# Optimization experiments

Measured on AMD Instinct MI355X. Metric: run time of the kernel, lower is better.

The kernel has to match this reference:

```python
import jax, jax.numpy as jnp
import numpy as np
from itertools import combinations

BASIS = 16  # identity + sums over every nonempty subset of the 4 set axes


def eq4_layer(x, coefs, bias):
    """Permutation-equivariant 4->4 set layer.
    x: (B, Din, n, n, n, n); coefs: (Din, Dout, 16); bias: (Dout,)
    Basis op 0 is identity; ops 1..15 are sums over each nonempty subset of the
    four set axes, broadcast back to full shape. We never stack the 16 full-size
    ops: pooled ops are contracted in their small (keepdims) form and broadcast-added.
    """
    out = jnp.einsum('ds,bdijkl->bsijkl', coefs[:, :, 0], x)
    b = 1
    for r in range(1, 5):
        for axes in combinations((2, 3, 4, 5), r):
            m = x.sum(axis=axes, keepdims=True)  # small marginal tensor
            out = out + jnp.einsum('ds,bd...->bs...', coefs[:, :, b], m)
            b += 1
    return out + bias.reshape(1, -1, 1, 1, 1, 1)


def setup_inputs() -> dict:
    key = jax.random.key(0)
    ks = jax.random.split(key, 9)
    B, n = 4, 24
    nembed, embed_dim, hid, out_dim = 1000, 15, 16, 16
    D = embed_dim + 1  # 16, = layers[0]
    s = 0.1
    return {
        'xcat': jax.random.randint(ks[0], (B, n), 0, nembed),
        'xfeat': jax.random.normal(ks[1], (B, n), dtype=jnp.float32),
        'embed': jax.random.normal(ks[2], (nembed, embed_dim), dtype=jnp.float32) * s,
        'coefs1': jax.random.normal(ks[3], (D, hid, BASIS), dtype=jnp.float32) * s,
        'bias1': jnp.zeros((hid,), dtype=jnp.float32),
        'coefs2': jax.random.normal(ks[4], (hid, out_dim, BASIS), dtype=jnp.float32) * s,
        'bias2': jnp.zeros((out_dim,), dtype=jnp.float32),
        'w_out': jax.random.normal(ks[5], (1, out_dim), dtype=jnp.float32) * s,
        'b_out': jnp.zeros((1,), dtype=jnp.float32),
    }


def reference(xcat, xfeat, embed, coefs1, bias1, coefs2, bias2, w_out, b_out):
    e = jax.nn.relu(embed[xcat])                       # (B, n, embed_dim)
    x = jnp.concatenate([e, xfeat[..., None]], axis=-1)  # (B, n, D)
    # 4th-order outer product per channel: (B, D, n, n, n, n)
    T = jnp.einsum('bid,bjd,bkd,bld->bdijkl', x, x, x, x)
    T = jax.nn.relu(eq4_layer(T, coefs1, bias1))
    T = jax.nn.relu(eq4_layer(T, coefs2, bias2))
    pooled = T.sum(axis=(2, 3, 4, 5))                  # (B, out_dim)
    return pooled @ w_out.T + b_out                    # (B, 1)
```

## Files before the change

### kernel.cpp

```cpp
#include <hip/hip_runtime.h>
#include <hip/hip_bf16.h>


#define NB 4
#define NN 24
#define ND 16
#define NS 16
#define NO 16
#define NKL 576
#define TSTRIDE 1152

typedef unsigned int u32;
typedef unsigned short u16;

__device__ __forceinline__ u16 f2bf(float f) {
  u32 u = __float_as_uint(f);
  u = (u + 0x7fffu + ((u >> 16) & 1u)) >> 16;
  return (u16)u;
}
__device__ __forceinline__ float bflo(u32 u) { return __uint_as_float(u << 16); }
__device__ __forceinline__ float bfhi(u32 u) { return __uint_as_float(u & 0xffff0000u); }

__global__ __launch_bounds__(256) void kt_tables(
    const int* __restrict__ xcat, const float* __restrict__ xfeat,
    const float* __restrict__ embed,
    const float* __restrict__ coefs1, const float* __restrict__ bias1,
    float* __restrict__ tabs) {
  const int blk = blockIdx.x;
  const int j = blk % NN, i = (blk / NN) % NN, b = blk / (NN * NN);
  const int t = threadIdx.x;
  __shared__ float sx[NN * ND];
  __shared__ float SwL[16];
  __shared__ float Af[256], tb[256], tg[256], td[256];
  __shared__ float dconst[16];
  for (int idx = t; idx < NN * ND; idx += 256) {
    int d = idx & 15, ii = idx >> 4;
    float v;
    if (d < 15) v = fmaxf(embed[xcat[b * NN + ii] * 15 + d], 0.f);
    else        v = xfeat[b * NN + ii];
    sx[idx] = v;
  }
  __syncthreads();
  if (t < 16) {
    float s = 0.f;
    for (int ii = 0; ii < NN; ++ii) s += sx[ii * 16 + t];
    SwL[t] = s;
  }
  __syncthreads();
  {
    int d = t >> 4, s = t & 15;
    const float* c = coefs1 + t * 16;
    float xi = sx[i * 16 + d], xj = sx[j * 16 + d];
    float Sv = SwL[d];
    float S2 = Sv * Sv, S3 = S2 * Sv, S4 = S2 * S2, pij = xi * xj;
    Af[s * 16 + d] = c[0] * pij + c[1] * Sv * xj + c[2] * Sv * xi + c[5] * S2;
    tb[t] = c[4] * Sv * pij + c[9] * S2 * xi + c[7] * S2 * xj + c[12] * S3;
    tg[t] = c[3] * Sv * pij + c[8] * S2 * xi + c[6] * S2 * xj + c[11] * S3;
    td[t] = c[10] * S2 * pij + c[14] * S3 * xi + c[13] * S3 * xj + c[15] * S4;
  }
  __syncthreads();
  if (t < 16) {
    float sd = 0.f;
    for (int d = 0; d < 16; ++d) sd += td[d * 16 + t];
    dconst[t] = sd + bias1[t];
  }
  __syncthreads();
  float* tile = tabs + (size_t)blk * TSTRIDE;
  if (t < 128) {
    int s = t >> 3, m = t & 7;
    tile[t] = __uint_as_float((u32)f2bf(Af[s * 16 + 2 * m]) |
                              ((u32)f2bf(Af[s * 16 + 2 * m + 1]) << 16));
  }
  for (int idx = t; idx < 768; idx += 256) {
    int pos = idx >> 4, s = idx & 15;
    if (pos < NN) {
      float acc = 0.f;
#pragma unroll
      for (int d = 0; d < 16; ++d) acc += tb[d * 16 + s] * sx[pos * 16 + d];
      tile[128 + s * 32 + (pos / 3) * 4 + pos % 3] = acc;
    } else {
      int l = pos - NN;
      float acc = dconst[s];
#pragma unroll
      for (int d = 0; d < 16; ++d) acc += tg[d * 16 + s] * sx[l * 16 + d];
      tile[640 + s * 32 + (l / 3) * 4 + l % 3] = acc;
    }
  }
}

__global__ __launch_bounds__(192, 2) void kb_eval(
    const int* __restrict__ xcat, const float* __restrict__ xfeat,
    const float* __restrict__ embed, const float* __restrict__ coefs2,
    const float* __restrict__ tabs,
    u32* __restrict__ T1g, u32* __restrict__ mkc_p, u32* __restrict__ mlc_p,
    u32* __restrict__ mklc_p) {
  const int blk = blockIdx.x;
  const int b = blk / (NN * NN);
  const int t = threadIdx.x;
  __shared__ float sx[NN * ND];
  __shared__ __align__(16) float tabL[TSTRIDE];
  __shared__ u32 T1p[NKL][9];
  __shared__ __align__(16) float rk[NN][20], rl[NN][20];
  __shared__ __align__(16) float rkl[16];
  __shared__ __align__(16) float c2kT[16][20], c2lT[16][20], c2qT[16][20];

  for (int idx = t; idx < NN * ND; idx += 192) {
    int d = idx & 15, ii = idx >> 4;
    float v;
    if (d < 15) v = fmaxf(embed[xcat[b * NN + ii] * 15 + d], 0.f);
    else        v = xfeat[b * NN + ii];
    sx[idx] = v;
  }
  for (int idx = t; idx < 288; idx += 192)
    ((float4*)tabL)[idx] = ((const float4*)(tabs + (size_t)blk * TSTRIDE))[idx];
  for (int idx = t; idx < 256; idx += 192) {
    int s = idx >> 4, s2 = idx & 15;
    c2kT[s2][s] = coefs2[idx * 16 + 3];
    c2lT[s2][s] = coefs2[idx * 16 + 4];
    c2qT[s2][s] = coefs2[idx * 16 + 10];
  }
  __syncthreads();

  const int grp = t >> 3, sub = t & 7, vr = 3 * sub;
  const int grpPos = (grp / 3) * 4 + grp % 3;
  float P0[16], P1[16], P2[16];
#pragma unroll
  for (int d = 0; d < 16; ++d) {
    float xc = sx[grp * 16 + d];
    P0[d] = sx[vr * 16 + d] * xc;
    P1[d] = sx[(vr + 1) * 16 + d] * xc;
    P2[d] = sx[(vr + 2) * 16 + d] * xc;
  }
  float pr0[16], pr1[16], pr2[16];
#pragma unroll
  for (int s = 0; s < 16; ++s) {
    const uint4* ap = (const uint4*)(tabL + s * 8);
    uint4 A0 = ap[0], A1 = ap[1];
    u32 qa[8] = {A0.x, A0.y, A0.z, A0.w, A1.x, A1.y, A1.z, A1.w};
    float Afr[16];
#pragma unroll
    for (int m = 0; m < 8; ++m) {
      Afr[2 * m] = bflo(qa[m]);
      Afr[2 * m + 1] = bfhi(qa[m]);
    }
    float4 vb4 = *(const float4*)(tabL + 128 + s * 32 + sub * 4);
    float ct = tabL[640 + s * 32 + grpPos];
    float v0 = vb4.x + ct, v1 = vb4.y + ct, v2 = vb4.z + ct;
#pragma unroll
    for (int d = 0; d < 16; ++d) {
      v0 += Afr[d] * P0[d];
      v1 += Afr[d] * P1[d];
      v2 += Afr[d] * P2[d];
    }
    pr0[s] = fmaxf(v0, 0.f);
    pr1[s] = fmaxf(v1, 0.f);
    pr2[s] = fmaxf(v2, 0.f);
  }
  const int klA = vr * NN + grp;
  auto emit = [&](float (&pr)[16], int kl) {
    u32 w[8];
#pragma unroll
    for (int m = 0; m < 8; ++m) {
      w[m] = (u32)f2bf(pr[2 * m]) | ((u32)f2bf(pr[2 * m + 1]) << 16);
      T1p[kl][m] = w[m];
    }
    uint4* gp = (uint4*)(T1g + ((size_t)blk * NKL + kl) * 8);
    gp[0] = make_uint4(w[0], w[1], w[2], w[3]);
    gp[1] = make_uint4(w[4], w[5], w[6], w[7]);
  };
  emit(pr0, klA); emit(pr1, klA + NN); emit(pr2, klA + 2 * NN);
  __syncthreads();

  for (int idx = t; idx < NN * NS; idx += 192) {
    int a = idx >> 4, s = idx & 15, m = s >> 1;
    u32 odd = (u32)(s & 1);
    float sk = 0.f, sl = 0.f;
    for (int c = 0; c < NN; ++c) {
      u32 uk = T1p[c * NN + a][m];
      u32 ul = T1p[a * NN + c][m];
      sk += odd ? bfhi(uk) : bflo(uk);
      sl += odd ? bfhi(ul) : bflo(ul);
    }
    rk[a][s] = sk;
    rl[a][s] = sl;
  }
  __syncthreads();
  if (t < 16) {
    float v = 0.f;
    for (int a = 0; a < NN; ++a) v += rk[a][t];
    rkl[t] = v;
  }
  __syncthreads();
  for (int idx = t; idx < 392; idx += 192) {
    int m = idx & 7, pos = idx >> 3;
    const float* raw; const float (*cT)[20]; u32* dst;
    if (pos < NN)           { raw = rk[pos];      cT = c2kT; dst = mkc_p + ((size_t)blk * NN + pos) * 8 + m; }
    else if (pos < 2 * NN)  { raw = rl[pos - NN]; cT = c2lT; dst = mlc_p + ((size_t)blk * NN + (pos - NN)) * 8 + m; }
    else                    { raw = rkl;          cT = c2qT; dst = mklc_p + (size_t)blk * 8 + m; }
    float o0 = 0.f, o1 = 0.f;
#pragma unroll
    for (int w = 0; w < 4; ++w) {
      float4 rv = ((const float4*)raw)[w];
      float4 m0 = ((const float4*)(&cT[2 * m][0]))[w];
      float4 m1 = ((const float4*)(&cT[2 * m + 1][0]))[w];
      o0 += rv.x * m0.x + rv.y * m0.y + rv.z * m0.z + rv.w * m0.w;
      o1 += rv.x * m1.x + rv.y * m1.y + rv.z * m1.z + rv.w * m1.w;
    }
    *dst = (u32)f2bf(o0) | ((u32)f2bf(o1) << 16);
  }
}

__global__ __launch_bounds__(256) void k3_marg(
    const u32* __restrict__ T1g, const float* __restrict__ coefs2,
    float* __restrict__ mi_raw, float* __restrict__ mj_raw,
    u32* __restrict__ mic_p, u32* __restrict__ mjc_p,
    float* __restrict__ quad_part) {
  const int t = threadIdx.x, bb = blockIdx.x;
  const int pos = bb * 256 + t;
  const bool isI = pos < 55296;
  const int p = isI ? pos : pos - 55296;
  __shared__ __align__(16) float ccT[16][20];
  __shared__ float qred[4][16];
  {
    int s = t >> 4, s2 = t & 15;
    ccT[s2][s] = coefs2[t * 16 + (isI ? 1 : 2)];
  }
  __syncthreads();
  const int ba = p / NKL, kl = p % NKL;
  const int b = ba / NN, a = ba % NN;
  const u32* base; size_t stride;
  if (isI) { base = T1g + ((size_t)(b * NN * NN + a) * NKL + kl) * 8; stride = (size_t)NN * NKL * 8; }
  else     { base = T1g + ((size_t)((b * NN + a) * NN) * NKL + kl) * 8; stride = (size_t)NKL * 8; }
  float raw[16];
#pragma unroll
  for (int s = 0; s < 16; ++s) raw[s] = 0.f;
  for (int c = 0; c < NN; ++c) {
    const uint4* q = (const uint4*)(base + c * stride);
    uint4 q0 = q[0], q1 = q[1];
    u32 qa[8] = {q0.x, q0.y, q0.z, q0.w, q1.x, q1.y, q1.z, q1.w};
#pragma unroll
    for (int m = 0; m < 8; ++m) {
      raw[2 * m] += bflo(qa[m]);
      raw[2 * m + 1] += bfhi(qa[m]);
    }
  }
  float* rdst = (isI ? mi_raw : mj_raw) + (size_t)p * 16;
#pragma unroll
  for (int w = 0; w < 4; ++w)
    ((float4*)rdst)[w] = make_float4(raw[4 * w], raw[4 * w + 1], raw[4 * w + 2], raw[4 * w + 3]);
  u32 op[8];
#pragma unroll
  for (int m = 0; m < 8; ++m) {
    float o0 = 0.f, o1 = 0.f;
#pragma unroll
    for (int w = 0; w < 4; ++w) {
      float4 m0 = ((const float4*)(&ccT[2 * m][0]))[w];
      float4 m1 = ((const float4*)(&ccT[2 * m + 1][0]))[w];
      o0 += m0.x * raw[4 * w] + m0.y * raw[4 * w + 1] + m0.z * raw[4 * w + 2] + m0.w * raw[4 * w + 3];
      o1 += m1.x * raw[4 * w] + m1.y * raw[4 * w + 1] + m1.z * raw[4 * w + 2] + m1.w * raw[4 * w + 3];
    }
    op[m] = (u32)f2bf(o0) | ((u32)f2bf(o1) << 16);
  }
  uint4* cdst = (uint4*)((isI ? mic_p : mjc_p) + (size_t)p * 8);
  cdst[0] = make_uint4(op[0], op[1], op[2], op[3]);
  cdst[1] = make_uint4(op[4], op[5], op[6], op[7]);
  if (isI) {
#pragma unroll
    for (int s = 0; s < 16; ++s) {
      float v = raw[s];
      for (int off = 32; off; off >>= 1) v += __shfl_xor(v, off, 64);
      raw[s] = v;
    }
    if ((t & 63) == 0) {
      int w = t >> 6;
#pragma unroll
      for (int s = 0; s < 16; ++s) qred[w][s] = raw[s];
    }
  }
  __syncthreads();
  if (isI && t < 16)
    quad_part[bb * 16 + t] = qred[0][t] + qred[1][t] + qred[2][t] + qred[3][t];
}

__global__ __launch_bounds__(256) void kd_derived(
    const float* __restrict__ mi_raw, const float* __restrict__ mj_raw,
    const float* __restrict__ quad_part, const float* __restrict__ coefs2,
    float* __restrict__ mijc, float* __restrict__ mikc, float* __restrict__ milc,
    float* __restrict__ mjkc, float* __restrict__ mjlc,
    float* __restrict__ mijkc, float* __restrict__ mijlc,
    float* __restrict__ miklc, float* __restrict__ mjklc,
    float* __restrict__ mijklc) {
  const int bb = blockIdx.x, t = threadIdx.x;
  __shared__ float cc[256];
  __shared__ float ex[16][17];
  __shared__ float tot[16];
  __shared__ float qr[64];
  if (bb < 720) {
    int tbl = bb / 144;
    cc[t] = coefs2[t * 16 + 5 + tbl];
    int pp = t >> 4, s = t & 15;
    int pos = (bb % 144) * 16 + pp;
    int b = pos / 576, rem = pos % 576;
    const float* srcb; int stride;
    if (tbl == 0) { srcb = mi_raw + ((size_t)b * 24 * 576 + rem) * 16 + s; stride = 576 * 16; }
    else if (tbl == 1) { int jj = rem / 24, l = rem % 24;
      srcb = mi_raw + (((size_t)(b * 24 + jj)) * 576 + l) * 16 + s; stride = 24 * 16; }
    else if (tbl == 2) { int jj = rem / 24, k = rem % 24;
      srcb = mi_raw + (((size_t)(b * 24 + jj)) * 576 + k * 24) * 16 + s; stride = 16; }
    else if (tbl == 3) { int ii = rem / 24, l = rem % 24;
      srcb = mj_raw + (((size_t)(b * 24 + ii)) * 576 + l) * 16 + s; stride = 24 * 16; }
    else { int ii = rem / 24, k = rem % 24;
      srcb = mj_raw + (((size_t)(b * 24 + ii)) * 576 + k * 24) * 16 + s; stride = 16; }
    float v = 0.f;
#pragma unroll 4
    for (int x = 0; x < 24; ++x) v += srcb[(size_t)x * stride];
    ex[pp][s] = v;
    __syncthreads();
    float o = 0.f;
#pragma unroll
    for (int ss = 0; ss < 16; ++ss) o += cc[ss * 16 + s] * ex[pp][ss];
    float* dst = (tbl == 0 ? mijc : tbl == 1 ? mikc : tbl == 2 ? milc : tbl == 3 ? mjkc : mjlc);
    dst[(size_t)pos * 16 + s] = o;
    return;
  }
  if (bb < 720 + 384) {
    int idx = bb - 720;
    int tbl = idx / 96, rr = idx % 96;
    int b = rr / 24, a = rr % 24;
    cc[t] = coefs2[t * 16 + 11 + tbl];
    int gg = t >> 4, s = t & 15;
    const float* src = (tbl == 3 ? mj_raw : mi_raw);
    float v = 0.f;
#pragma unroll 4
    for (int m = 0; m < 36; ++m) {
      int u = gg + (m << 4);
      size_t addr;
      if (tbl == 0) { int j = u / 24, k = u % 24;
        addr = (((size_t)(b * 24 + j)) * 576 + k * 24 + a) * 16 + s; }
      else if (tbl == 1) { int j = u / 24, l = u % 24;
        addr = (((size_t)(b * 24 + j)) * 576 + a * 24 + l) * 16 + s; }
      else {
        addr = (((size_t)(b * 24 + a)) * 576 + u) * 16 + s; }
      v += src[addr];
    }
    ex[gg][s] = v;
    __syncthreads();
    if (t < 16) {
      float w2 = 0.f;
#pragma unroll
      for (int g2 = 0; g2 < 16; ++g2) w2 += ex[g2][t];
      tot[t] = w2;
    }
    __syncthreads();
    if (t < 16) {
      float o = 0.f;
#pragma unroll
      for (int ss = 0; ss < 16; ++ss) o += cc[ss * 16 + t] * tot[ss];
      float* dst = (tbl == 0 ? mijkc : tbl == 1 ? mijlc : tbl == 2 ? miklc : mjklc);
      dst[(size_t)(b * 24 + a) * 16 + t] = o;
    }
    return;
  }
  if (t < 64) {
    int b = t >> 4, s = t & 15;
    float v = 0.f;
    for (int c = 0; c < 54; ++c) v += quad_part[(b * 54 + c) * 16 + s];
    qr[t] = v;
  }
  __syncthreads();
  if (t < 64) {
    int b = t >> 4, s2 = t & 15;
    float o = 0.f;
#pragma unroll
    for (int s = 0; s < 16; ++s) o += coefs2[(s * 16 + s2) * 16 + 15] * qr[b * 16 + s];
    mijklc[t] = o;
  }
}

__global__ __launch_bounds__(192, 2) void k5_final(
    const u32* __restrict__ T1g,
    const u32* __restrict__ mic_p, const u32* __restrict__ mjc_p,
    const u32* __restrict__ mkc_p, const u32* __restrict__ mlc_p,
    const u32* __restrict__ mklc_p,
    const float* __restrict__ mijc, const float* __restrict__ mikc,
    const float* __restrict__ milc, const float* __restrict__ mjkc,
    const float* __restrict__ mjlc,
    const float* __restrict__ mijkc, const float* __restrict__ mijlc,
    const float* __restrict__ miklc, const float* __restrict__ mjklc,
    const float* __restrict__ mijklc,
    const float* __restrict__ coefs2, const float* __restrict__ bias2,
    const float* __restrict__ w_out, float* __restrict__ pool_part) {
  const int orig = blockIdx.x;
  const int blk = (orig & 7) * 288 + (orig >> 3);
  const int j = blk % NN, i2 = (blk / NN) % NN, b = blk / (NN * NN);
  const int t = threadIdx.x;
  __shared__ __align__(16) u32 c2p[128];
  __shared__ __align__(16) float Kt[NN][16], Lt[NN][16];
  __shared__ __align__(16) float cterm[16], wl[16];
  __shared__ float wsum[3];

  if (t < 128) {
    int s = t >> 3, m = t & 7;
    c2p[t] = (u32)f2bf(coefs2[(s * 16 + 2 * m) * 16]) |
             ((u32)f2bf(coefs2[(s * 16 + 2 * m + 1) * 16]) << 16);
  }
  for (int idx = t; idx < NN * NO; idx += 192) {
    int kk = idx >> 4, s2 = idx & 15, m = s2 >> 1;
    u32 odd = (u32)(s2 & 1);
    u32 ul = mlc_p[((size_t)blk * NN + kk) * 8 + m];
    u32 uk = mkc_p[((size_t)blk * NN + kk) * 8 + m];
    Kt[kk][s2] = (odd ? bfhi(ul) : bflo(ul))
               + mjlc[(size_t)((b * NN + i2) * NN + kk) * NS + s2]
               + milc[(size_t)((b * NN + j) * NN + kk) * NS + s2]
               + mijlc[(size_t)(b * NN + kk) * NS + s2];
    Lt[kk][s2] = (odd ? bfhi(uk) : bflo(uk))
               + mjkc[(size_t)((b * NN + i2) * NN + kk) * NS + s2]
               + mikc[(size_t)((b * NN + j) * NN + kk) * NS + s2]
               + mijkc[(size_t)(b * NN + kk) * NS + s2];
  }
  if (t < NO) {
    u32 uq = mklc_p[(size_t)blk * 8 + (t >> 1)];
    cterm[t] = ((t & 1) ? bfhi(uq) : bflo(uq))
             + miklc[(size_t)(b * NN + j) * NS + t]
             + mjklc[(size_t)(b * NN + i2) * NS + t]
             + mijklc[(size_t)b * NS + t] + bias2[t];
    wl[t] = w_out[t];
  }
  __syncthreads();

  u32 qa0[8], qa1[8], qa2[8];
  float acc0[16], acc1[16], acc2[16];
  auto loadElem = [&](int c, u32 (&qa)[8], float (&acc)[16]) {
    const int kl = t + 192 * c;
    const int k = kl / NN, l = kl % NN;
    const uint4* pt = (const uint4*)(T1g + ((size_t)blk * NKL + kl) * 8);
    const uint4* pi = (const uint4*)(mic_p + ((size_t)((b * NN + j) * NKL + kl)) * 8);
    const uint4* pj = (const uint4*)(mjc_p + ((size_t)((b * NN + i2) * NKL + kl)) * 8);
    const float4* ps = (const float4*)(mijc + ((size_t)(b * NKL + kl)) * 16);
    uint4 t0 = pt[0], t1 = pt[1];
    uint4 i0 = pi[0], i1 = pi[1];
    uint4 j0 = pj[0], j1 = pj[1];
    float4 s0 = ps[0], s1 = ps[1], s2v = ps[2], s3 = ps[3];
    qa[0] = t0.x; qa[1] = t0.y; qa[2] = t0.z; qa[3] = t0.w;
    qa[4] = t1.x; qa[5] = t1.y; qa[6] = t1.z; qa[7] = t1.w;
    u32 ia[8] = {i0.x, i0.y, i0.z, i0.w, i1.x, i1.y, i1.z, i1.w};
    u32 ja[8] = {j0.x, j0.y, j0.z, j0.w, j1.x, j1.y, j1.z, j1.w};
    float sv[16];
    ((float4*)sv)[0] = s0; ((float4*)sv)[1] = s1; ((float4*)sv)[2] = s2v; ((float4*)sv)[3] = s3;
#pragma unroll
    for (int m = 0; m < 8; ++m) {
      acc[2 * m]     = cterm[2 * m]     + Kt[k][2 * m]     + Lt[l][2 * m]
                     + bflo(ia[m]) + bflo(ja[m]) + sv[2 * m];
      acc[2 * m + 1] = cterm[2 * m + 1] + Kt[k][2 * m + 1] + Lt[l][2 * m + 1]
                     + bfhi(ia[m]) + bfhi(ja[m]) + sv[2 * m + 1];
    }
  };
  loadElem(0, qa0, acc0); loadElem(1, qa1, acc1); loadElem(2, qa2, acc2);

#pragma unroll
  for (int s = 0; s < 16; ++s) {
    const uint4* cp = (const uint4*)(c2p + s * 8);
    uint4 C0 = cp[0], C1 = cp[1];
    u32 ca[8] = {C0.x, C0.y, C0.z, C0.w, C1.x, C1.y, C1.z, C1.w};
    float row[16];
#pragma unroll
    for (int m = 0; m < 8; ++m) {
      row[2 * m] = bflo(ca[m]);
      row[2 * m + 1] = bfhi(ca[m]);
    }
    float v0 = (s & 1) ? bfhi(qa0[s >> 1]) : bflo(qa0[s >> 1]);
    float v1 = (s & 1) ? bfhi(qa1[s >> 1]) : bflo(qa1[s >> 1]);
    float v2 = (s & 1) ? bfhi(qa2[s >> 1]) : bflo(qa2[s >> 1]);
#pragma unroll
    for (int s2 = 0; s2 < 16; ++s2) {
      acc0[s2] += row[s2] * v0;
      acc1[s2] += row[s2] * v1;
      acc2[s2] += row[s2] * v2;
    }
  }
  float p = 0.f;
#pragma unroll
  for (int s2 = 0; s2 < 16; ++s2)
    p += wl[s2] * (fmaxf(acc0[s2], 0.f) + fmaxf(acc1[s2], 0.f) + fmaxf(acc2[s2], 0.f));
  for (int off = 32; off; off >>= 1) p += __shfl_down(p, off, 64);
  if ((t & 63) == 0) wsum[t >> 6] = p;
  __syncthreads();
  if (t == 0) pool_part[blk] = wsum[0] + wsum[1] + wsum[2];
}

__global__ __launch_bounds__(256) void k6_out(
    const float* __restrict__ pool_part, const float* __restrict__ b_out,
    float* __restrict__ out) {
  const int t = threadIdx.x;
  const int b = t >> 6, lane = t & 63;
  float v = 0.f;
  for (int c = lane; c < 576; c += 64) v += pool_part[b * 576 + c];
  for (int off = 32; off; off >>= 1) v += __shfl_down(v, off, 64);
  if (lane == 0) out[b] = v + b_out[0];
}

extern "C" void kernel_launch(void* const* d_in, const int* in_sizes, int n_in,
                              void* d_out, int out_size, void* d_ws, size_t ws_size,
                              hipStream_t stream) {
  (void)in_sizes; (void)n_in; (void)out_size; (void)ws_size;
  const int*   xcat   = (const int*)d_in[0];
  const float* xfeat  = (const float*)d_in[1];
  const float* embed  = (const float*)d_in[2];
  const float* coefs1 = (const float*)d_in[3];
  const float* bias1  = (const float*)d_in[4];
  const float* coefs2 = (const float*)d_in[5];
  const float* bias2  = (const float*)d_in[6];
  const float* w_out  = (const float*)d_in[7];
  const float* b_out  = (const float*)d_in[8];
  float* out = (float*)d_out;
  char* ws = (char*)d_ws;

  u32*   T1g      = (u32*)(ws + 0);
  float* tabs     = (float*)(ws + 42467328);
  float* mi_raw   = (float*)(ws + 42467328);
  float* mj_raw   = (float*)(ws + 46006272);
  u32*   mic_p    = (u32*)(ws + 49545216);
  u32*   mjc_p    = (u32*)(ws + 51314688);
  u32*   mkc_p    = (u32*)(ws + 53084160);
  u32*   mlc_p    = (u32*)(ws + 54853632);
  u32*   mklc_p   = (u32*)(ws + 56623104);
  float* mijc     = (float*)(ws + 56696832);
  float* mikc     = (float*)(ws + 56844288);
  float* milc     = (float*)(ws + 56991744);
  float* mjkc     = (float*)(ws + 57139200);
  float* mjlc     = (float*)(ws + 57286656);
  float* mijkc    = (float*)(ws + 57434112);
  float* mijlc    = (float*)(ws + 57440256);
  float* miklc    = (float*)(ws + 57446400);
  float* mjklc    = (float*)(ws + 57452544);
  float* mijklc   = (float*)(ws + 57458688);
  float* quad_part= (float*)(ws + 57458944);
  float* pool_part= (float*)(ws + 57472768);

  kt_tables<<<NB * NN * NN, 256, 0, stream>>>(xcat, xfeat, embed, coefs1, bias1, tabs);
  kb_eval<<<NB * NN * NN, 192, 0, stream>>>(xcat, xfeat, embed, coefs2, tabs,
                                            T1g, mkc_p, mlc_p, mklc_p);
  k3_marg<<<432, 256, 0, stream>>>(T1g, coefs2, mi_raw, mj_raw, mic_p, mjc_p, quad_part);
  kd_derived<<<1105, 256, 0, stream>>>(mi_raw, mj_raw, quad_part, coefs2,
                                       mijc, mikc, milc, mjkc, mjlc,
                                       mijkc, mijlc, miklc, mjklc, mijklc);
  k5_final<<<NB * NN * NN, 192, 0, stream>>>(T1g, mic_p, mjc_p, mkc_p, mlc_p, mklc_p,
                                             mijc, mikc, milc, mjkc, mjlc,
                                             mijkc, mijlc, miklc, mjklc, mijklc,
                                             coefs2, bias2, w_out, pool_part);
  k6_out<<<1, 256, 0, stream>>>(pool_part, b_out, out);
}
```

Baseline: 105.1 us.

## Fuse table-building kernel into kb_eval and store i/j marginals as packed bf16

Removes the separate kt_tables launch: each kb_eval block now computes its per-(b,i,j) coefficient tables directly into shared memory instead of writing them to global memory and reading them back. The raw i/j marginals produced by k3_marg are now stored as packed bf16 pairs instead of fp32, which halves their traffic in kd_derived. kd_derived's block mapping is rewritten to handle two channels per thread, cutting its grid size. The trade-offs are more table math on the 192-thread blocks, extra shared memory pressure in kb_eval, and lower precision in the second-level marginals.

Result: faster. 101.3 us (-3.6%).

```diff
diff --git a/kernel.cpp b/kernel.cpp
--- a/kernel.cpp
+++ b/kernel.cpp
@@ -21,11 +21,13 @@
 __device__ __forceinline__ float bflo(u32 u) { return __uint_as_float(u << 16); }
 __device__ __forceinline__ float bfhi(u32 u) { return __uint_as_float(u & 0xffff0000u); }
 
-__global__ __launch_bounds__(256) void kt_tables(
+__global__ __launch_bounds__(192, 2) void kb_eval(
     const int* __restrict__ xcat, const float* __restrict__ xfeat,
     const float* __restrict__ embed,
     const float* __restrict__ coefs1, const float* __restrict__ bias1,
-    float* __restrict__ tabs) {
+    const float* __restrict__ coefs2,
+    u32* __restrict__ T1g, u32* __restrict__ mkc_p, u32* __restrict__ mlc_p,
+    u32* __restrict__ mklc_p) {
   const int blk = blockIdx.x;
   const int j = blk % NN, i = (blk / NN) % NN, b = blk / (NN * NN);
   const int t = threadIdx.x;
@@ -33,71 +35,6 @@
   __shared__ float SwL[16];
   __shared__ float Af[256], tb[256], tg[256], td[256];
   __shared__ float dconst[16];
-  for (int idx = t; idx < NN * ND; idx += 256) {
-    int d = idx & 15, ii = idx >> 4;
-    float v;
-    if (d < 15) v = fmaxf(embed[xcat[b * NN + ii] * 15 + d], 0.f);
-    else        v = xfeat[b * NN + ii];
-    sx[idx] = v;
-  }
-  __syncthreads();
-  if (t < 16) {
-    float s = 0.f;
-    for (int ii = 0; ii < NN; ++ii) s += sx[ii * 16 + t];
-    SwL[t] = s;
-  }
-  __syncthreads();
-  {
-    int d = t >> 4, s = t & 15;
-    const float* c = coefs1 + t * 16;
-    float xi = sx[i * 16 + d], xj = sx[j * 16 + d];
-    float Sv = SwL[d];
-    float S2 = Sv * Sv, S3 = S2 * Sv, S4 = S2 * S2, pij = xi * xj;
-    Af[s * 16 + d] = c[0] * pij + c[1] * Sv * xj + c[2] * Sv * xi + c[5] * S2;
-    tb[t] = c[4] * Sv * pij + c[9] * S2 * xi + c[7] * S2 * xj + c[12] * S3;
-    tg[t] = c[3] * Sv * pij + c[8] * S2 * xi + c[6] * S2 * xj + c[11] * S3;
-    td[t] = c[10] * S2 * pij + c[14] * S3 * xi + c[13] * S3 * xj + c[15] * S4;
-  }
-  __syncthreads();
-  if (t < 16) {
-    float sd = 0.f;
-    for (int d = 0; d < 16; ++d) sd += td[d * 16 + t];
-    dconst[t] = sd + bias1[t];
-  }
-  __syncthreads();
-  float* tile = tabs + (size_t)blk * TSTRIDE;
-  if (t < 128) {
-    int s = t >> 3, m = t & 7;
-    tile[t] = __uint_as_float((u32)f2bf(Af[s * 16 + 2 * m]) |
-                              ((u32)f2bf(Af[s * 16 + 2 * m + 1]) << 16));
-  }
-  for (int idx = t; idx < 768; idx += 256) {
-    int pos = idx >> 4, s = idx & 15;
-    if (pos < NN) {
-      float acc = 0.f;
-#pragma unroll
-      for (int d = 0; d < 16; ++d) acc += tb[d * 16 + s] * sx[pos * 16 + d];
-      tile[128 + s * 32 + (pos / 3) * 4 + pos % 3] = acc;
-    } else {
-      int l = pos - NN;
-      float acc = dconst[s];
-#pragma unroll
-      for (int d = 0; d < 16; ++d) acc += tg[d * 16 + s] * sx[l * 16 + d];
-      tile[640 + s * 32 + (l / 3) * 4 + l % 3] = acc;
-    }
-  }
-}
-
-__global__ __launch_bounds__(192, 2) void kb_eval(
-    const int* __restrict__ xcat, const float* __restrict__ xfeat,
-    const float* __restrict__ embed, const float* __restrict__ coefs2,
-    const float* __restrict__ tabs,
-    u32* __restrict__ T1g, u32* __restrict__ mkc_p, u32* __restrict__ mlc_p,
-    u32* __restrict__ mklc_p) {
-  const int blk = blockIdx.x;
-  const int b = blk / (NN * NN);
-  const int t = threadIdx.x;
-  __shared__ float sx[NN * ND];
   __shared__ __align__(16) float tabL[TSTRIDE];
   __shared__ u32 T1p[NKL][9];
   __shared__ __align__(16) float rk[NN][20], rl[NN][20];
@@ -111,13 +48,56 @@
     else        v = xfeat[b * NN + ii];
     sx[idx] = v;
   }
-  for (int idx = t; idx < 288; idx += 192)
-    ((float4*)tabL)[idx] = ((const float4*)(tabs + (size_t)blk * TSTRIDE))[idx];
   for (int idx = t; idx < 256; idx += 192) {
     int s = idx >> 4, s2 = idx & 15;
     c2kT[s2][s] = coefs2[idx * 16 + 3];
     c2lT[s2][s] = coefs2[idx * 16 + 4];
     c2qT[s2][s] = coefs2[idx * 16 + 10];
+  }
+  __syncthreads();
+  if (t < 16) {
+    float s = 0.f;
+    for (int ii = 0; ii < NN; ++ii) s += sx[ii * 16 + t];
+    SwL[t] = s;
+  }
+  __syncthreads();
+  for (int idx = t; idx < 256; idx += 192) {
+    int d = idx >> 4, s = idx & 15;
+    const float* c = coefs1 + idx * 16;
+    float xi = sx[i * 16 + d], xj = sx[j * 16 + d];
+    float Sv = SwL[d];
+    float S2 = Sv * Sv, S3 = S2 * Sv, S4 = S2 * S2, pij = xi * xj;
+    Af[s * 16 + d] = c[0] * pij + c[1] * Sv * xj + c[2] * Sv * xi + c[5] * S2;
+    tb[idx] = c[4] * Sv * pij + c[9] * S2 * xi + c[7] * S2 * xj + c[12] * S3;
+    tg[idx] = c[3] * Sv * pij + c[8] * S2 * xi + c[6] * S2 * xj + c[11] * S3;
+    td[idx] = c[10] * S2 * pij + c[14] * S3 * xi + c[13] * S3 * xj + c[15] * S4;
+  }
+  __syncthreads();
+  if (t < 16) {
+    float sd = 0.f;
+    for (int d = 0; d < 16; ++d) sd += td[d * 16 + t];
+    dconst[t] = sd + bias1[t];
+  }
+  __syncthreads();
+  if (t < 128) {
+    int s = t >> 3, m = t & 7;
+    tabL[t] = __uint_as_float((u32)f2bf(Af[s * 16 + 2 * m]) |
+                              ((u32)f2bf(Af[s * 16 + 2 * m + 1]) << 16));
+  }
+  for (int idx = t; idx < 768; idx += 192) {
+    int pos = idx >> 4, s = idx & 15;
+    if (pos < NN) {
+      float acc = 0.f;
+#pragma unroll
+      for (int d = 0; d < 16; ++d) acc += tb[d * 16 + s] * sx[pos * 16 + d];
+      tabL[128 + s * 32 + (pos / 3) * 4 + pos % 3] = acc;
+    } else {
+      int l = pos - NN;
+      float acc = dconst[s];
+#pragma unroll
+      for (int d = 0; d < 16; ++d) acc += tg[d * 16 + s] * sx[l * 16 + d];
+      tabL[640 + s * 32 + (l / 3) * 4 + l % 3] = acc;
+    }
   }
   __syncthreads();
 
@@ -212,7 +192,7 @@
 
 __global__ __launch_bounds__(256) void k3_marg(
     const u32* __restrict__ T1g, const float* __restrict__ coefs2,
-    float* __restrict__ mi_raw, float* __restrict__ mj_raw,
+    u32* __restrict__ mi_p, u32* __restrict__ mj_p,
     u32* __restrict__ mic_p, u32* __restrict__ mjc_p,
     float* __restrict__ quad_part) {
   const int t = threadIdx.x, bb = blockIdx.x;
@@ -244,13 +224,10 @@
       raw[2 * m + 1] += bfhi(qa[m]);
     }
   }
-  float* rdst = (isI ? mi_raw : mj_raw) + (size_t)p * 16;
-#pragma unroll
-  for (int w = 0; w < 4; ++w)
-    ((float4*)rdst)[w] = make_float4(raw[4 * w], raw[4 * w + 1], raw[4 * w + 2], raw[4 * w + 3]);
-  u32 op[8];
+  u32 rp[8], op[8];
 #pragma unroll
   for (int m = 0; m < 8; ++m) {
+    rp[m] = (u32)f2bf(raw[2 * m]) | ((u32)f2bf(raw[2 * m + 1]) << 16);
     float o0 = 0.f, o1 = 0.f;
 #pragma unroll
     for (int w = 0; w < 4; ++w) {
@@ -261,6 +238,9 @@
     }
     op[m] = (u32)f2bf(o0) | ((u32)f2bf(o1) << 16);
   }
+  uint4* rdst = (uint4*)((isI ? mi_p : mj_p) + (size_t)p * 8);
+  rdst[0] = make_uint4(rp[0], rp[1], rp[2], rp[3]);
+  rdst[1] = make_uint4(rp[4], rp[5], rp[6], rp[7]);
   uint4* cdst = (uint4*)((isI ? mic_p : mjc_p) + (size_t)p * 8);
   cdst[0] = make_uint4(op[0], op[1], op[2], op[3]);
   cdst[1] = make_uint4(op[4], op[5], op[6], op[7]);
@@ -283,7 +263,7 @@
 }
 
 __global__ __launch_bounds__(256) void kd_derived(
-    const float* __restrict__ mi_raw, const float* __restrict__ mj_raw,
+    const u32* __restrict__ mi_p, const u32* __restrict__ mj_p,
     const float* __restrict__ quad_part, const float* __restrict__ coefs2,
     float* __restrict__ mijc, float* __restrict__ mikc, float* __restrict__ milc,
     float* __restrict__ mjkc, float* __restrict__ mjlc,
@@ -292,63 +272,72 @@
     float* __restrict__ mijklc) {
   const int bb = blockIdx.x, t = threadIdx.x;
   __shared__ float cc[256];
-  __shared__ float ex[16][17];
+  __shared__ float ex[32][17];
   __shared__ float tot[16];
   __shared__ float qr[64];
-  if (bb < 720) {
-    int tbl = bb / 144;
+  if (bb < 360) {
+    int tbl = bb / 72;
     cc[t] = coefs2[t * 16 + 5 + tbl];
-    int pp = t >> 4, s = t & 15;
-    int pos = (bb % 144) * 16 + pp;
+    int pp = t >> 3, m = t & 7;
+    int pos = (bb % 72) * 32 + pp;
     int b = pos / 576, rem = pos % 576;
-    const float* srcb; int stride;
-    if (tbl == 0) { srcb = mi_raw + ((size_t)b * 24 * 576 + rem) * 16 + s; stride = 576 * 16; }
+    const u32* srcb; int stride;
+    if (tbl == 0) { srcb = mi_p + ((size_t)b * 24 * 576 + rem) * 8 + m; stride = 576 * 8; }
     else if (tbl == 1) { int jj = rem / 24, l = rem % 24;
-      srcb = mi_raw + (((size_t)(b * 24 + jj)) * 576 + l) * 16 + s; stride = 24 * 16; }
+      srcb = mi_p + (((size_t)(b * 24 + jj)) * 576 + l) * 8 + m; stride = 24 * 8; }
     else if (tbl == 2) { int jj = rem / 24, k = rem % 24;
-      srcb = mi_raw + (((size_t)(b * 24 + jj)) * 576 + k * 24) * 16 + s; stride = 16; }
+      srcb = mi_p + (((size_t)(b * 24 + jj)) * 576 + k * 24) * 8 + m; stride = 8; }
     else if (tbl == 3) { int ii = rem / 24, l = rem % 24;
-      srcb = mj_raw + (((size_t)(b * 24 + ii)) * 576 + l) * 16 + s; stride = 24 * 16; }
+      srcb = mj_p + (((size_t)(b * 24 + ii)) * 576 + l) * 8 + m; stride = 24 * 8; }
     else { int ii = rem / 24, k = rem % 24;
-      srcb = mj_raw + (((size_t)(b * 24 + ii)) * 576 + k * 24) * 16 + s; stride = 16; }
-    float v = 0.f;
+      srcb = mj_p + (((size_t)(b * 24 + ii)) * 576 + k * 24) * 8 + m; stride = 8; }
+    float v0 = 0.f, v1 = 0.f;
 #pragma unroll 4
-    for (int x = 0; x < 24; ++x) v += srcb[(size_t)x * stride];
-    ex[pp][s] = v;
+    for (int x = 0; x < 24; ++x) {
+      u32 u = srcb[(size_t)x * stride];
+      v0 += bflo(u); v1 += bfhi(u);
+    }
+    ex[pp][2 * m] = v0;
+    ex[pp][2 * m + 1] = v1;
     __syncthreads();
-    float o = 0.f;
-#pragma unroll
-    for (int ss = 0; ss < 16; ++ss) o += cc[ss * 16 + s] * ex[pp][ss];
     float* dst = (tbl == 0 ? mijc : tbl == 1 ? mikc : tbl == 2 ? milc : tbl == 3 ? mjkc : mjlc);
-    dst[(size_t)pos * 16 + s] = o;
+    for (int idx = t; idx < 512; idx += 256) {
+      int pp2 = idx >> 4, s2 = idx & 15;
+      float o = 0.f;
+#pragma unroll
+      for (int ss = 0; ss < 16; ++ss) o += cc[ss * 16 + s2] * ex[pp2][ss];
+      dst[(size_t)((bb % 72) * 32 + pp2) * 16 + s2] = o;
+    }
     return;
   }
-  if (bb < 720 + 384) {
-    int idx = bb - 720;
+  if (bb < 360 + 384) {
+    int idx = bb - 360;
     int tbl = idx / 96, rr = idx % 96;
     int b = rr / 24, a = rr % 24;
     cc[t] = coefs2[t * 16 + 11 + tbl];
-    int gg = t >> 4, s = t & 15;
-    const float* src = (tbl == 3 ? mj_raw : mi_raw);
-    float v = 0.f;
-#pragma unroll 4
-    for (int m = 0; m < 36; ++m) {
-      int u = gg + (m << 4);
+    int gg = t >> 3, m = t & 7;
+    const u32* src = (tbl == 3 ? mj_p : mi_p);
+    float v0 = 0.f, v1 = 0.f;
+#pragma unroll 2
+    for (int it = 0; it < 18; ++it) {
+      int u = gg + (it << 5);
       size_t addr;
       if (tbl == 0) { int j = u / 24, k = u % 24;
-        addr = (((size_t)(b * 24 + j)) * 576 + k * 24 + a) * 16 + s; }
+        addr = (((size_t)(b * 24 + j)) * 576 + k * 24 + a) * 8 + m; }
       else if (tbl == 1) { int j = u / 24, l = u % 24;
-        addr = (((size_t)(b * 24 + j)) * 576 + a * 24 + l) * 16 + s; }
+        addr = (((size_t)(b * 24 + j)) * 576 + a * 24 + l) * 8 + m; }
       else {
-        addr = (((size_t)(b * 24 + a)) * 576 + u) * 16 + s; }
-      v += src[addr];
-    }
-    ex[gg][s] = v;
+        addr = (((size_t)(b * 24 + a)) * 576 + u) * 8 + m; }
+      u32 uu = src[addr];
+      v0 += bflo(uu); v1 += bfhi(uu);
+    }
+    ex[gg][2 * m] = v0;
+    ex[gg][2 * m + 1] = v1;
     __syncthreads();
     if (t < 16) {
       float w2 = 0.f;
 #pragma unroll
-      for (int g2 = 0; g2 < 16; ++g2) w2 += ex[g2][t];
+      for (int g2 = 0; g2 < 32; ++g2) w2 += ex[g2][t];
       tot[t] = w2;
     }
     __syncthreads();
@@ -516,34 +505,32 @@
   char* ws = (char*)d_ws;
 
   u32*   T1g      = (u32*)(ws + 0);
-  float* tabs     = (float*)(ws + 42467328);
-  float* mi_raw   = (float*)(ws + 42467328);
-  float* mj_raw   = (float*)(ws + 46006272);
-  u32*   mic_p    = (u32*)(ws + 49545216);
-  u32*   mjc_p    = (u32*)(ws + 51314688);
-  u32*   mkc_p    = (u32*)(ws + 53084160);
-  u32*   mlc_p    = (u32*)(ws + 54853632);
-  u32*   mklc_p   = (u32*)(ws + 56623104);
-  float* mijc     = (float*)(ws + 56696832);
-  float* mikc     = (float*)(ws + 56844288);
-  float* milc     = (float*)(ws + 56991744);
-  float* mjkc     = (float*)(ws + 57139200);
-  float* mjlc     = (float*)(ws + 57286656);
-  float* mijkc    = (float*)(ws + 57434112);
-  float* mijlc    = (float*)(ws + 57440256);
-  float* miklc    = (float*)(ws + 57446400);
-  float* mjklc    = (float*)(ws + 57452544);
-  float* mijklc   = (float*)(ws + 57458688);
-  float* quad_part= (float*)(ws + 57458944);
-  float* pool_part= (float*)(ws + 57472768);
-
-  kt_tables<<<NB * NN * NN, 256, 0, stream>>>(xcat, xfeat, embed, coefs1, bias1, tabs);
-  kb_eval<<<NB * NN * NN, 192, 0, stream>>>(xcat, xfeat, embed, coefs2, tabs,
-                                            T1g, mkc_p, mlc_p, mklc_p);
-  k3_marg<<<432, 256, 0, stream>>>(T1g, coefs2, mi_raw, mj_raw, mic_p, mjc_p, quad_part);
-  kd_derived<<<1105, 256, 0, stream>>>(mi_raw, mj_raw, quad_part, coefs2,
-                                       mijc, mikc, milc, mjkc, mjlc,
-                                       mijkc, mijlc, miklc, mjklc, mijklc);
+  u32*   mi_p     = (u32*)(ws + 42467328);
+  u32*   mj_p     = (u32*)(ws + 44236800);
+  u32*   mic_p    = (u32*)(ws + 46006272);
+  u32*   mjc_p    = (u32*)(ws + 47775744);
+  u32*   mkc_p    = (u32*)(ws + 49545216);
+  u32*   mlc_p    = (u32*)(ws + 51314688);
+  u32*   mklc_p   = (u32*)(ws + 53084160);
+  float* mijc     = (float*)(ws + 53157888);
+  float* mikc     = (float*)(ws + 53305344);
+  float* milc     = (float*)(ws + 53452800);
+  float* mjkc     = (float*)(ws + 53600256);
+  float* mjlc     = (float*)(ws + 53747712);
+  float* mijkc    = (float*)(ws + 53895168);
+  float* mijlc    = (float*)(ws + 53901312);
+  float* miklc    = (float*)(ws + 53907456);
+  float* mjklc    = (float*)(ws + 53913600);
+  float* mijklc   = (float*)(ws + 53919744);
+  float* quad_part= (float*)(ws + 53920000);
+  float* pool_part= (float*)(ws + 53933824);
+
+  kb_eval<<<NB * NN * NN, 192, 0, stream>>>(xcat, xfeat, embed, coefs1, bias1,
+                                            coefs2, T1g, mkc_p, mlc_p, mklc_p);
+  k3_marg<<<432, 256, 0, stream>>>(T1g, coefs2, mi_p, mj_p, mic_p, mjc_p, quad_part);
+  kd_derived<<<745, 256, 0, stream>>>(mi_p, mj_p, quad_part, coefs2,
+                                      mijc, mikc, milc, mjkc, mjlc,
+                                      mijkc, mijlc, miklc, mjklc, mijklc);
   k5_final<<<NB * NN * NN, 192, 0, stream>>>(T1g, mic_p, mjc_p, mkc_p, mlc_p, mklc_p,
                                              mijc, mikc, milc, mjkc, mjlc,
                                              mijkc, mijlc, miklc, mjklc, mijklc,
```
